# Kernel tuning notes

Hardware: AMD Instinct MI355X
Metric: run time of the kernel (lower is better)

The kernel has to match this reference:

```python
import jax, jax.numpy as jnp
import numpy as np

B, QL, KVL = 2, 1024, 2048
D = 4096          # hidden_size
NH, NKV = 32, 8   # attention heads / kv heads
HD = D // NH      # head_dim = 128
INNER = 4 * D     # SwiGLU intermediate = 16384
EPS = 1e-5
THETA = 10000.0


def rope_cos_sin(seq_len, head_dim, theta):
    inv_freq = 1.0 / (theta ** (jnp.arange(0, head_dim, 2, dtype=jnp.float32) / head_dim))
    t = jnp.arange(seq_len, dtype=jnp.float32)
    freqs = jnp.outer(t, inv_freq)                      # [S, HD/2]
    emb = jnp.concatenate([freqs, freqs], axis=-1)      # [S, HD]
    return jnp.cos(emb), jnp.sin(emb)


def rotate_half(x):
    half = x.shape[-1] // 2
    return jnp.concatenate([-x[..., half:], x[..., :half]], axis=-1)


def apply_rope(x, cos, sin):
    # x: [B, H, S, HD]; cos/sin: [S, HD] broadcast over batch & heads
    return x * cos[None, None] + rotate_half(x) * sin[None, None]


def layernorm(x, w, b):
    mu = jnp.mean(x, axis=-1, keepdims=True)
    var = jnp.var(x, axis=-1, keepdims=True)
    return (x - mu) * jax.lax.rsqrt(var + EPS) * w + b


def setup_inputs() -> dict:
    key = jax.random.key(0)
    ks = jax.random.split(key, 12)
    s = 0.02
    return {
        "hidden_states": jax.random.normal(ks[0], (B, QL, D), jnp.float32),
        "encoder_hidden_states": jax.random.normal(ks[1], (B, KVL, D), jnp.float32),
        "encoder_attention_mask": jnp.ones((B, KVL), jnp.float32),
        "ln1_w": jnp.ones((D,), jnp.float32),
        "ln1_b": jnp.zeros((D,), jnp.float32),
        "q_w": jax.random.normal(ks[2], (D, D), jnp.float32) * s,        # [out, in]
        "k_w": jax.random.normal(ks[3], (NKV * HD, D), jnp.float32) * s,
        "v_w": jax.random.normal(ks[4], (NKV * HD, D), jnp.float32) * s,
        "o_w": jax.random.normal(ks[5], (D, D), jnp.float32) * s,
        "ln2_w": jnp.ones((D,), jnp.float32),
        "ln2_b": jnp.zeros((D,), jnp.float32),
        "gate_w": jax.random.normal(ks[6], (INNER, D), jnp.float32) * s,
        "up_w": jax.random.normal(ks[7], (INNER, D), jnp.float32) * s,
        "down_w": jax.random.normal(ks[8], (D, INNER), jnp.float32) * s,
    }


def reference(hidden_states, encoder_hidden_states, encoder_attention_mask,
              ln1_w, ln1_b, q_w, k_w, v_w, o_w, ln2_w, ln2_b,
              gate_w, up_w, down_w):
    residual = hidden_states
    h = layernorm(hidden_states, ln1_w, ln1_b)

    # projections
    q = (h @ q_w.T).reshape(B, QL, NH, HD).transpose(0, 2, 1, 3)                    # [B,NH,QL,HD]
    k = (encoder_hidden_states @ k_w.T).reshape(B, KVL, NKV, HD).transpose(0, 2, 1, 3)  # [B,NKV,KVL,HD]
    v = (encoder_hidden_states @ v_w.T).reshape(B, KVL, NKV, HD).transpose(0, 2, 1, 3)

    # RoPE: q uses positions 0..QL-1, k uses positions 0..KVL-1 (position_ids=None -> cos[None])
    q_cos, q_sin = rope_cos_sin(QL, HD, THETA)
    kv_cos, kv_sin = rope_cos_sin(KVL, HD, THETA)
    q = apply_rope(q, q_cos, q_sin)
    k = apply_rope(k, kv_cos, kv_sin)

    # GQA repeat_kv: each kv head repeated num_key_value_groups times consecutively
    n_rep = NH // NKV
    k = jnp.repeat(k, n_rep, axis=1)  # [B,NH,KVL,HD]
    v = jnp.repeat(v, n_rep, axis=1)

    attn = jnp.einsum('bhqd,bhkd->bhqk', q, k) / np.sqrt(HD).astype(np.float32)
    # NOTE: original code ADDS the boolean mask (True -> +1.0) to the logits
    mask = (encoder_attention_mask != 0).astype(attn.dtype)  # [B,KVL]
    attn = attn + mask[:, None, None, :]
    attn = jax.nn.softmax(attn.astype(jnp.float32), axis=-1).astype(q.dtype)

    out = jnp.einsum('bhqk,bhkd->bhqd', attn, v)        # [B,NH,QL,HD]
    out = out.transpose(0, 2, 1, 3).reshape(B, QL, D)
    attn_out = out @ o_w.T

    h = residual + attn_out
    residual = h
    h = layernorm(h, ln2_w, ln2_b)
    ff = (jax.nn.silu(h @ gate_w.T) * (h @ up_w.T)) @ down_w.T
    return residual + ff
```

## Files before the change

### kernel.cpp

```cpp
#include <hip/hip_runtime.h>
#include <hip/hip_bf16.h>
#include <math.h>

using bf16 = __hip_bfloat16;
typedef __bf16 bfv8 __attribute__((ext_vector_type(8)));
typedef float f32x4 __attribute__((ext_vector_type(4)));

__device__ __forceinline__ f32x4 mfma16(bfv8 a, bfv8 b, f32x4 c) {
    return __builtin_amdgcn_mfma_f32_16x16x32_bf16(a, b, c, 0, 0, 0);
}

__device__ __forceinline__ void gload_lds16(const void* g, void* l) {
    __builtin_amdgcn_global_load_lds(
        (const __attribute__((address_space(1))) void*)g,
        (__attribute__((address_space(3))) void*)l, 16, 0, 0);
}

__global__ void cvt_kernel(const float* __restrict__ in, bf16* __restrict__ out, long n8) {
    long u = (long)blockIdx.x * 256 + threadIdx.x;
    if (u >= n8) return;
    const float4* p = (const float4*)in + u * 2;
    float4 a = p[0], b = p[1];
    bf16 t8[8] = { __float2bfloat16(a.x), __float2bfloat16(a.y), __float2bfloat16(a.z), __float2bfloat16(a.w),
                   __float2bfloat16(b.x), __float2bfloat16(b.y), __float2bfloat16(b.z), __float2bfloat16(b.w) };
    *(int4*)(out + u * 8) = *(const int4*)t8;
}

__global__ void layernorm_kernel(const float* __restrict__ x, const float* __restrict__ gw,
                                 const float* __restrict__ gb, bf16* __restrict__ out)
{
    const int D = 4096;
    int row = blockIdx.x, t = threadIdx.x;
    const float4* xr = (const float4*)(x + (size_t)row * D);
    float4 v[4];
    float s1 = 0.f, s2 = 0.f;
#pragma unroll
    for (int j = 0; j < 4; ++j) {
        v[j] = xr[t + j * 256];
        s1 += v[j].x + v[j].y + v[j].z + v[j].w;
        s2 += v[j].x * v[j].x + v[j].y * v[j].y + v[j].z * v[j].z + v[j].w * v[j].w;
    }
#pragma unroll
    for (int d = 1; d < 64; d <<= 1) { s1 += __shfl_xor(s1, d); s2 += __shfl_xor(s2, d); }
    __shared__ float red[8];
    int wave = t >> 6, lane = t & 63;
    if (lane == 0) { red[wave] = s1; red[4 + wave] = s2; }
    __syncthreads();
    s1 = red[0] + red[1] + red[2] + red[3];
    s2 = red[4] + red[5] + red[6] + red[7];
    float mu = s1 * (1.f / 4096.f);
    float var = s2 * (1.f / 4096.f) - mu * mu;
    float rs = rsqrtf(var + 1e-5f);
    bf16* orow = out + (size_t)row * D;
#pragma unroll
    for (int j = 0; j < 4; ++j) {
        int base = (t + j * 256) * 4;
        float xs[4] = { v[j].x, v[j].y, v[j].z, v[j].w };
        bf16 o4[4];
#pragma unroll
        for (int c = 0; c < 4; ++c)
            o4[c] = __float2bfloat16((xs[c] - mu) * rs * gw[base + c] + gb[base + c]);
        *(int2*)(orow + base) = *(const int2*)o4;
    }
}

__global__ void rope_kernel(bf16* __restrict__ x, int nheads, int seqlen, long total) {
    long idx = (long)blockIdx.x * 256 + threadIdx.x;
    if (idx >= total) return;
    int j = (int)(idx & 63);
    long t2 = idx >> 6;
    int h = (int)(t2 % nheads);
    long row = t2 / nheads;
    int pos = (int)(row % seqlen);
    float inv = exp2f(-(float)j * 0.20762050593046015f);
    float ang = (float)pos * inv;
    float s, c;
    sincosf(ang, &s, &c);
    bf16* p = x + row * ((long)nheads * 128) + (long)h * 128 + j;
    float x0 = __bfloat162float(p[0]);
    float x1 = __bfloat162float(p[64]);
    p[0]  = __float2bfloat16(x0 * c - x1 * s);
    p[64] = __float2bfloat16(x1 * c + x0 * s);
}

template<int BM, int BN, int MODE, bool DUAL, int CM, int CN, int XN>
__global__ __launch_bounds__(512, 2) void gemm_p(
        const bf16* __restrict__ A, const bf16* __restrict__ W, const bf16* __restrict__ W2,
        void* __restrict__ Cout, void* __restrict__ Cout2, const void* __restrict__ aux,
        int M, int N, int K, int Nsplit)
{
    constexpr int MF = BM / 32;
    constexpr int NF = BN / 64;
    constexpr int ALD = BM / 128;
    constexpr int BLD = BN / 128;
    constexpr int SLD = ALD + BLD;
    __shared__ bf16 lds[3][(BM + BN) * 32];

    const int t = threadIdx.x;
    const int wid = t >> 6, lane = t & 63;
    const int lr = lane & 15, lg = lane >> 4;
    const int wr = wid >> 2, wc = wid & 3;
    const int bid = blockIdx.x;
    const int xcd = bid & 7, slot = bid >> 3;
    const int sm = slot / CN, sn = slot % CN;
    const int xm = xcd / XN, xn = xcd % XN;
    const int bm = (xm * CM + sm) * BM;
    const int bn = (xn * CN + sn) * BN;

    auto stage = [&](int tt, int buf) {
        const int k0 = tt * 32;
        char* ldsA = (char*)&lds[buf][0];
#pragma unroll
        for (int c = 0; c < ALD; ++c) {
            int Wb = (t + c * 512) * 16;
            int L = Wb ^ (((Wb >> 7) & 7) << 4);
            int row = L >> 6, colb = L & 63;
            gload_lds16(A + (size_t)(bm + row) * K + k0 + (colb >> 1), ldsA + Wb);
        }
        char* ldsB = (char*)&lds[buf][BM * 32];
#pragma unroll
        for (int c = 0; c < BLD; ++c) {
            int Wb = (t + c * 512) * 16;
            int L = Wb ^ (((Wb >> 7) & 7) << 4);
            int row = L >> 6, colb = L & 63;
            const bf16* src;
            if constexpr (DUAL) {
                int nr = bn + row;
                src = (nr >= Nsplit) ? W2 + (size_t)(nr - Nsplit) * K + k0 + (colb >> 1)
                                     : W  + (size_t)nr * K + k0 + (colb >> 1);
            } else {
                src = W + (size_t)(bn + row) * K + k0 + (colb >> 1);
            }
            gload_lds16(src, ldsB + Wb);
        }
    };

    const f32x4 zero4 = { 0.f, 0.f, 0.f, 0.f };
    f32x4 acc[MF][NF];
#pragma unroll
    for (int m = 0; m < MF; ++m)
#pragma unroll
        for (int n = 0; n < NF; ++n) acc[m][n] = zero4;

    const int T = K >> 5;
    stage(0, 0);
    stage(1, 1);
    if constexpr (SLD == 4) asm volatile("s_waitcnt vmcnt(4)" ::: "memory");
    else                    asm volatile("s_waitcnt vmcnt(3)" ::: "memory");
    __builtin_amdgcn_s_barrier();
    __builtin_amdgcn_sched_barrier(0);

    for (int tt = 0; tt < T; ++tt) {
        const int buf = tt % 3;
        bfv8 af[MF], bfr[NF];
#pragma unroll
        for (int m = 0; m < MF; ++m) {
            int row = wr * (BM / 2) + m * 16 + lr;
            int U = row * 64 + lg * 16;
            af[m] = *(const bfv8*)((const char*)&lds[buf][0] + (U ^ (((U >> 7) & 7) << 4)));
        }
#pragma unroll
        for (int n = 0; n < NF; ++n) {
            int row = wc * (BN / 4) + n * 16 + lr;
            int U = row * 64 + lg * 16;
            bfr[n] = *(const bfv8*)((const char*)&lds[buf][BM * 32] + (U ^ (((U >> 7) & 7) << 4)));
        }
        if (tt + 2 < T) stage(tt + 2, (tt + 2) % 3);
        __builtin_amdgcn_s_setprio(1);
#pragma unroll
        for (int m = 0; m < MF; ++m)
#pragma unroll
            for (int n = 0; n < NF; ++n)
                acc[m][n] = mfma16(af[m], bfr[n], acc[m][n]);
        __builtin_amdgcn_s_setprio(0);
        if (tt + 2 < T) {
            if constexpr (SLD == 4) asm volatile("s_waitcnt vmcnt(4)" ::: "memory");
            else                    asm volatile("s_waitcnt vmcnt(3)" ::: "memory");
        } else {
            asm volatile("s_waitcnt vmcnt(0)" ::: "memory");
        }
        __builtin_amdgcn_s_barrier();
        __builtin_amdgcn_sched_barrier(0);
    }

    const int r0 = bm + wr * (BM / 2), c0 = bn + wc * (BN / 4);
#pragma unroll
    for (int m = 0; m < MF; ++m)
#pragma unroll
        for (int n = 0; n < NF; ++n)
#pragma unroll
            for (int i = 0; i < 4; ++i) {
                int r = r0 + m * 16 + lg * 4 + i;
                int c = c0 + n * 16 + lr;
                float a = acc[m][n][i];
                if constexpr (DUAL) {
                    if (c < Nsplit) ((bf16*)Cout)[(size_t)r * Nsplit + c] = __float2bfloat16(a);
                    else ((bf16*)Cout2)[(size_t)r * (N - Nsplit) + (c - Nsplit)] = __float2bfloat16(a);
                } else {
                    size_t idx = (size_t)r * N + c;
                    if constexpr (MODE == 0) {
                        ((bf16*)Cout)[idx] = __float2bfloat16(a);
                    } else if constexpr (MODE == 1) {
                        a = a / (1.f + expf(-a));
                        ((bf16*)Cout)[idx] = __float2bfloat16(a);
                    } else if constexpr (MODE == 2) {
                        a *= __bfloat162float(((const bf16*)aux)[idx]);
                        ((bf16*)Cout)[idx] = __float2bfloat16(a);
                    } else {
                        ((float*)Cout)[idx] = a + ((const float*)aux)[idx];
                    }
                }
            }
}

__global__ void transpose_v(const bf16* __restrict__ vb, bf16* __restrict__ vt) {
    __shared__ bf16 tile[64][68];
    int kv0 = blockIdx.x * 64, c0 = blockIdx.y * 64, b = blockIdx.z;
    int t = threadIdx.x;
    int cr = t & 15, rr = t >> 4;
#pragma unroll
    for (int j = 0; j < 4; ++j) {
        int r = rr + j * 16;
        *(int2*)&tile[r][cr * 4] = *(const int2*)&vb[(size_t)(b * 2048 + kv0 + r) * 1024 + c0 + cr * 4];
    }
    __syncthreads();
#pragma unroll
    for (int j = 0; j < 4; ++j) {
        int cc = rr + j * 16;
        bf16 tmp[4];
#pragma unroll
        for (int q = 0; q < 4; ++q) tmp[q] = tile[cr * 4 + q][cc];
        *(int2*)&vt[(size_t)(b * 1024 + c0 + cc) * 2048 + kv0 + cr * 4] = *(const int2*)tmp;
    }
}

__global__ __launch_bounds__(256) void attn_kernel(
    const bf16* __restrict__ Q, const bf16* __restrict__ Kb, const bf16* __restrict__ Vt,
    const float* __restrict__ mask, bf16* __restrict__ O)
{
    const int QL_ = 1024, KVL_ = 2048;
    const float scale = 0.08838834764831845f;
    int qt = blockIdx.x, h = blockIdx.y, b = blockIdx.z;
    int t = threadIdx.x, wave = t >> 6, lane = t & 63;
    int lr = lane & 15, lg = lane >> 4;
    int g = h >> 2;
    __shared__ bf16 Ksm[64 * 128];
    __shared__ bf16 Vsm[128 * 64];
    __shared__ bf16 Psm[4][16 * 72];
    int q0 = qt * 64 + wave * 16;

    const bf16* qptr = Q + (size_t)(b * QL_ + q0 + lr) * 4096 + h * 128;
    bfv8 qf[4];
#pragma unroll
    for (int kc = 0; kc < 4; ++kc) qf[kc] = *(const bfv8*)(qptr + kc * 32 + lg * 8);

    const f32x4 zero4 = { 0.f, 0.f, 0.f, 0.f };
    f32x4 accO[8];
#pragma unroll
    for (int dt = 0; dt < 8; ++dt) accO[dt] = zero4;
    float mrow[4] = { -1e30f, -1e30f, -1e30f, -1e30f };
    float lrow[4] = { 0.f, 0.f, 0.f, 0.f };

    for (int kv0 = 0; kv0 < KVL_; kv0 += 64) {
#pragma unroll
        for (int p2 = 0; p2 < 4; ++p2) {
            int Wb = (p2 * 256 + t) * 16;
            int row = Wb >> 8;
            int col = ((Wb & 255) ^ ((row & 7) << 4)) >> 1;
            gload_lds16(Kb + (size_t)(b * KVL_ + kv0 + row) * 1024 + g * 128 + col,
                        (char*)Ksm + Wb);
        }
#pragma unroll
        for (int p2 = 0; p2 < 4; ++p2) {
            int Wb = (p2 * 256 + t) * 16;
            int row = Wb >> 7;
            int col = ((Wb & 127) ^ ((row & 7) << 4)) >> 1;
            gload_lds16(Vt + (size_t)(b * 1024 + g * 128 + row) * 2048 + kv0 + col,
                        (char*)Vsm + Wb);
        }
        __syncthreads();

        f32x4 s[4];
#pragma unroll
        for (int ct = 0; ct < 4; ++ct) {
            s[ct] = zero4;
#pragma unroll
            for (int kc = 0; kc < 4; ++kc) {
                int row = ct * 16 + lr;
                int U = row * 256 + kc * 64 + lg * 16;
                bfv8 kf = *(const bfv8*)((const char*)Ksm + (U ^ ((row & 7) << 4)));
                s[ct] = mfma16(qf[kc], kf, s[ct]);
            }
            float mv = mask[(size_t)b * KVL_ + kv0 + ct * 16 + lr];
            mv = (mv != 0.f) ? 1.f : 0.f;
#pragma unroll
            for (int i = 0; i < 4; ++i) s[ct][i] = s[ct][i] * scale + mv;
        }

        float rmx[4], mnew[4], corr[4], psum[4];
#pragma unroll
        for (int i = 0; i < 4; ++i) {
            rmx[i] = fmaxf(fmaxf(s[0][i], s[1][i]), fmaxf(s[2][i], s[3][i]));
#pragma unroll
            for (int d = 1; d < 16; d <<= 1) rmx[i] = fmaxf(rmx[i], __shfl_xor(rmx[i], d));
            mnew[i] = fmaxf(mrow[i], rmx[i]);
            corr[i] = expf(mrow[i] - mnew[i]);
            psum[i] = 0.f;
        }
#pragma unroll
        for (int ct = 0; ct < 4; ++ct)
#pragma unroll
            for (int i = 0; i < 4; ++i) {
                float pv = expf(s[ct][i] - mnew[i]);
                psum[i] += pv;
                Psm[wave][(lg * 4 + i) * 72 + ct * 16 + lr] = __float2bfloat16(pv);
            }
#pragma unroll
        for (int i = 0; i < 4; ++i) {
#pragma unroll
            for (int d = 1; d < 16; d <<= 1) psum[i] += __shfl_xor(psum[i], d);
            lrow[i] = lrow[i] * corr[i] + psum[i];
            mrow[i] = mnew[i];
        }
#pragma unroll
        for (int dt = 0; dt < 8; ++dt)
#pragma unroll
            for (int i = 0; i < 4; ++i) accO[dt][i] *= corr[i];
        __syncthreads();

        bfv8 pf0 = *(const bfv8*)&Psm[wave][lr * 72 + 0 * 32 + lg * 8];
        bfv8 pf1 = *(const bfv8*)&Psm[wave][lr * 72 + 1 * 32 + lg * 8];
#pragma unroll
        for (int dt = 0; dt < 8; ++dt) {
            int row = dt * 16 + lr;
            int U0 = row * 128 + 0 * 64 + lg * 16;
            int U1 = row * 128 + 1 * 64 + lg * 16;
            bfv8 vf0 = *(const bfv8*)((const char*)Vsm + (U0 ^ ((row & 7) << 4)));
            bfv8 vf1 = *(const bfv8*)((const char*)Vsm + (U1 ^ ((row & 7) << 4)));
            accO[dt] = mfma16(pf0, vf0, accO[dt]);
            accO[dt] = mfma16(pf1, vf1, accO[dt]);
        }
        __syncthreads();
    }

    float invl[4];
#pragma unroll
    for (int i = 0; i < 4; ++i) invl[i] = 1.f / lrow[i];
#pragma unroll
    for (int dt = 0; dt < 8; ++dt)
#pragma unroll
        for (int i = 0; i < 4; ++i)
            O[(size_t)(b * QL_ + q0 + lg * 4 + i) * 4096 + h * 128 + dt * 16 + lr] =
                __float2bfloat16(accO[dt][i] * invl[i]);
}

extern "C" void kernel_launch(void* const* d_in, const int* in_sizes, int n_in,
                              void* d_out, int out_size, void* d_ws, size_t ws_size,
                              hipStream_t stream) {
    const float* hidden = (const float*)d_in[0];
    const float* enc    = (const float*)d_in[1];
    const float* mask   = (const float*)d_in[2];
    const float* ln1w   = (const float*)d_in[3];
    const float* ln1b   = (const float*)d_in[4];
    const float* qw     = (const float*)d_in[5];
    const float* kw     = (const float*)d_in[6];
    const float* vw     = (const float*)d_in[7];
    const float* ow     = (const float*)d_in[8];
    const float* ln2w   = (const float*)d_in[9];
    const float* ln2b   = (const float*)d_in[10];
    const float* gatew  = (const float*)d_in[11];
    const float* upw    = (const float*)d_in[12];
    const float* downw  = (const float*)d_in[13];
    float* out = (float*)d_out;

    char* ws = (char*)d_ws;
    bf16*  wbuf  = (bf16*)(ws);
    bf16*  wbuf2 = (bf16*)(ws + 8388608);
    bf16*  h1    = (bf16*)(ws + 134217728);
    bf16*  encb  = (bf16*)(ws + 150994944);
    bf16*  qb    = (bf16*)(ws + 184549376);
    bf16*  kb    = (bf16*)(ws + 201326592);
    bf16*  vb    = (bf16*)(ws + 209715200);
    bf16*  attno = (bf16*)(ws + 218103808);
    float* h2    = (float*)(ws + 234881024);
    bf16*  vt    = (bf16*)(ws + 234881024);
    bf16*  h2n   = (bf16*)(ws + 268435456);
    bf16*  g1    = (bf16*)(ws + 285212672);

    auto cvt = [&](const float* src, bf16* dst, long n) {
        cvt_kernel<<<(int)(n / 2048), 256, 0, stream>>>(src, dst, n / 8);
    };

    cvt(enc, encb, 16777216L);
    layernorm_kernel<<<2048, 256, 0, stream>>>(hidden, ln1w, ln1b, h1);

    cvt(qw, wbuf, 16777216L);
    gemm_p<128, 256, 0, false, 8, 4, 4><<<256, 512, 0, stream>>>(
        h1, wbuf, nullptr, qb, nullptr, nullptr, 2048, 4096, 4096, 0);
    rope_kernel<<<16384, 256, 0, stream>>>(qb, 32, 1024, 2048L * 32 * 64);

    cvt(kw, wbuf, 4194304L);
    cvt(vw, wbuf2, 4194304L);
    gemm_p<128, 256, 0, true, 8, 4, 2><<<256, 512, 0, stream>>>(
        encb, wbuf, wbuf2, kb, vb, nullptr, 4096, 2048, 4096, 1024);
    rope_kernel<<<8192, 256, 0, stream>>>(kb, 8, 2048, 4096L * 8 * 64);
    transpose_v<<<dim3(32, 16, 2), 256, 0, stream>>>(vb, vt);

    attn_kernel<<<dim3(16, 32, 2), 256, 0, stream>>>(qb, kb, vt, mask, attno);

    cvt(ow, wbuf, 16777216L);
    gemm_p<128, 256, 3, false, 8, 4, 4><<<256, 512, 0, stream>>>(
        attno, wbuf, nullptr, h2, nullptr, hidden, 2048, 4096, 4096, 0);

    layernorm_kernel<<<2048, 256, 0, stream>>>(h2, ln2w, ln2b, h2n);

    cvt(gatew, wbuf, 67108864L);
    gemm_p<256, 256, 1, false, 8, 8, 8><<<512, 512, 0, stream>>>(
        h2n, wbuf, nullptr, g1, nullptr, nullptr, 2048, 16384, 4096, 0);
    cvt(upw, wbuf, 67108864L);
    gemm_p<256, 256, 2, false, 8, 8, 8><<<512, 512, 0, stream>>>(
        h2n, wbuf, nullptr, g1, nullptr, g1, 2048, 16384, 4096, 0);

    cvt(downw, wbuf, 67108864L);
    gemm_p<128, 256, 3, false, 8, 4, 4><<<256, 512, 0, stream>>>(
        g1, wbuf, nullptr, out, nullptr, h2, 2048, 4096, 16384, 0);
}
```

Before: 1.574 ms.

## Replace GEMM with 256-row, K=64 double-buffered 8-wave ping-pong schedule

Rewrites the bf16 MFMA GEMM into a kernel with fixed 256-row M tiles and 64-wide K steps in two LDS buffers. Each K step is split into four quadrant phases, with LDS fragment loads interleaved between barrier-separated MFMA bursts, and the next stage is prefetched mid-iteration. The aim is to overlap LDS reads and global loads with matrix math and to cut per-K-step barrier overhead. In exchange it uses more registers and LDS, drops occupancy to one block per CU, and changes the tile-to-block mapping, so the 128-BN launches now cover 256 rows per block.

```diff
diff --git a/kernel.cpp b/kernel.cpp
--- a/kernel.cpp
+++ b/kernel.cpp
@@ -83,18 +83,18 @@
     p[64] = __float2bfloat16(x1 * c + x0 * s);
 }
 
-template<int BM, int BN, int MODE, bool DUAL, int CM, int CN, int XN>
-__global__ __launch_bounds__(512, 2) void gemm_p(
+template<int BN, int MODE, bool DUAL, int CM, int CN, int XN>
+__global__ __launch_bounds__(512, 1) void gemm8(
         const bf16* __restrict__ A, const bf16* __restrict__ W, const bf16* __restrict__ W2,
         void* __restrict__ Cout, void* __restrict__ Cout2, const void* __restrict__ aux,
         int M, int N, int K, int Nsplit)
 {
-    constexpr int MF = BM / 32;
-    constexpr int NF = BN / 64;
-    constexpr int ALD = BM / 128;
-    constexpr int BLD = BN / 128;
-    constexpr int SLD = ALD + BLD;
-    __shared__ bf16 lds[3][(BM + BN) * 32];
+    constexpr int NFH = BN / 128;
+    constexpr int ABY = 256 * 128;
+    constexpr int BBY = BN * 128;
+    constexpr int BLD = BN / 64;
+    constexpr int SLD = 4 + BLD;
+    __shared__ alignas(16) char lds8[2][ABY + BBY];
 
     const int t = threadIdx.x;
     const int wid = t >> 6, lane = t & 63;
@@ -104,95 +104,132 @@
     const int xcd = bid & 7, slot = bid >> 3;
     const int sm = slot / CN, sn = slot % CN;
     const int xm = xcd / XN, xn = xcd % XN;
-    const int bm = (xm * CM + sm) * BM;
+    const int bm = (xm * CM + sm) * 256;
     const int bn = (xn * CN + sn) * BN;
 
-    auto stage = [&](int tt, int buf) {
-        const int k0 = tt * 32;
-        char* ldsA = (char*)&lds[buf][0];
-#pragma unroll
-        for (int c = 0; c < ALD; ++c) {
+    auto stage = [&](int kt, int b) {
+        const int k0 = kt * 64;
+        char* base = &lds8[b][0];
+#pragma unroll
+        for (int c = 0; c < 4; ++c) {
             int Wb = (t + c * 512) * 16;
             int L = Wb ^ (((Wb >> 7) & 7) << 4);
-            int row = L >> 6, colb = L & 63;
-            gload_lds16(A + (size_t)(bm + row) * K + k0 + (colb >> 1), ldsA + Wb);
-        }
-        char* ldsB = (char*)&lds[buf][BM * 32];
+            gload_lds16(A + (size_t)(bm + (L >> 7)) * K + k0 + ((L & 127) >> 1), base + Wb);
+        }
 #pragma unroll
         for (int c = 0; c < BLD; ++c) {
             int Wb = (t + c * 512) * 16;
             int L = Wb ^ (((Wb >> 7) & 7) << 4);
-            int row = L >> 6, colb = L & 63;
             const bf16* src;
             if constexpr (DUAL) {
-                int nr = bn + row;
-                src = (nr >= Nsplit) ? W2 + (size_t)(nr - Nsplit) * K + k0 + (colb >> 1)
-                                     : W  + (size_t)nr * K + k0 + (colb >> 1);
+                int nr = bn + (L >> 7);
+                src = (nr >= Nsplit) ? W2 + (size_t)(nr - Nsplit) * K + k0 + ((L & 127) >> 1)
+                                     : W  + (size_t)nr * K + k0 + ((L & 127) >> 1);
             } else {
-                src = W + (size_t)(bn + row) * K + k0 + (colb >> 1);
+                src = W + (size_t)(bn + (L >> 7)) * K + k0 + ((L & 127) >> 1);
             }
-            gload_lds16(src, ldsB + Wb);
+            gload_lds16(src, base + ABY + Wb);
         }
     };
 
     const f32x4 zero4 = { 0.f, 0.f, 0.f, 0.f };
-    f32x4 acc[MF][NF];
-#pragma unroll
-    for (int m = 0; m < MF; ++m)
-#pragma unroll
-        for (int n = 0; n < NF; ++n) acc[m][n] = zero4;
-
-    const int T = K >> 5;
+    f32x4 acc[8][2 * NFH];
+#pragma unroll
+    for (int m = 0; m < 8; ++m)
+#pragma unroll
+        for (int n = 0; n < 2 * NFH; ++n) acc[m][n] = zero4;
+
+    bfv8 af[4][2], bfr[2][NFH][2];
+
+#define LOADA(B, MH) do {                                                     \
+    const char* _ba = &lds8[B][0];                                            \
+    _Pragma("unroll") for (int m = 0; m < 4; ++m)                             \
+    _Pragma("unroll") for (int ks = 0; ks < 2; ++ks) {                        \
+        int row = wr * 128 + (MH) * 64 + m * 16 + lr;                         \
+        int U = row * 128 + ks * 64 + lg * 16;                                \
+        af[m][ks] = *(const bfv8*)(_ba + (U ^ ((row & 7) << 4)));             \
+    } } while (0)
+
+#define LOADB(B, NH) do {                                                     \
+    const char* _bb = &lds8[B][ABY];                                          \
+    _Pragma("unroll") for (int n = 0; n < NFH; ++n)                           \
+    _Pragma("unroll") for (int ks = 0; ks < 2; ++ks) {                        \
+        int row = wc * (BN / 4) + (NH) * (BN / 8) + n * 16 + lr;              \
+        int U = row * 128 + ks * 64 + lg * 16;                                \
+        bfr[NH][n][ks] = *(const bfv8*)(_bb + (U ^ ((row & 7) << 4)));        \
+    } } while (0)
+
+#define MFMAQ(MH, NH) do {                                                    \
+    _Pragma("unroll") for (int m = 0; m < 4; ++m)                             \
+    _Pragma("unroll") for (int n = 0; n < NFH; ++n) {                         \
+        acc[(MH)*4+m][(NH)*NFH+n] = mfma16(af[m][0], bfr[NH][n][0], acc[(MH)*4+m][(NH)*NFH+n]); \
+        acc[(MH)*4+m][(NH)*NFH+n] = mfma16(af[m][1], bfr[NH][n][1], acc[(MH)*4+m][(NH)*NFH+n]); \
+    } } while (0)
+
+#define PH_TOP() do { __builtin_amdgcn_sched_barrier(0); __builtin_amdgcn_s_barrier();       \
+    asm volatile("s_waitcnt lgkmcnt(0)" ::: "memory"); __builtin_amdgcn_sched_barrier(0);    \
+    __builtin_amdgcn_s_setprio(1); } while (0)
+
+#define PH_END() do { __builtin_amdgcn_s_setprio(0); __builtin_amdgcn_sched_barrier(0);      \
+    __builtin_amdgcn_s_barrier(); } while (0)
+
+#define VM_PRE() do { if constexpr (SLD == 8) asm volatile("s_waitcnt vmcnt(8)" ::: "memory"); \
+                      else asm volatile("s_waitcnt vmcnt(6)" ::: "memory"); } while (0)
+
+    const int T = K >> 6;
+    const int T2 = T >> 1;
+
     stage(0, 0);
     stage(1, 1);
-    if constexpr (SLD == 4) asm volatile("s_waitcnt vmcnt(4)" ::: "memory");
-    else                    asm volatile("s_waitcnt vmcnt(3)" ::: "memory");
+    VM_PRE();
+    __builtin_amdgcn_sched_barrier(0);
     __builtin_amdgcn_s_barrier();
-    __builtin_amdgcn_sched_barrier(0);
-
-    for (int tt = 0; tt < T; ++tt) {
-        const int buf = tt % 3;
-        bfv8 af[MF], bfr[NF];
-#pragma unroll
-        for (int m = 0; m < MF; ++m) {
-            int row = wr * (BM / 2) + m * 16 + lr;
-            int U = row * 64 + lg * 16;
-            af[m] = *(const bfv8*)((const char*)&lds[buf][0] + (U ^ (((U >> 7) & 7) << 4)));
-        }
-#pragma unroll
-        for (int n = 0; n < NF; ++n) {
-            int row = wc * (BN / 4) + n * 16 + lr;
-            int U = row * 64 + lg * 16;
-            bfr[n] = *(const bfv8*)((const char*)&lds[buf][BM * 32] + (U ^ (((U >> 7) & 7) << 4)));
-        }
-        if (tt + 2 < T) stage(tt + 2, (tt + 2) % 3);
-        __builtin_amdgcn_s_setprio(1);
-#pragma unroll
-        for (int m = 0; m < MF; ++m)
-#pragma unroll
-            for (int n = 0; n < NF; ++n)
-                acc[m][n] = mfma16(af[m], bfr[n], acc[m][n]);
+
+    for (int tt = 0; tt < T2; ++tt) {
+        const bool pre = (tt + 1 < T2);
+        LOADA(0, 0); LOADB(0, 0);
+        PH_TOP(); MFMAQ(0, 0); PH_END();
+        LOADB(0, 1);
+        PH_TOP(); MFMAQ(0, 1); PH_END();
+        LOADA(0, 1);
+        PH_TOP(); MFMAQ(1, 1); PH_END();
+        if (pre) stage(2 * tt + 2, 0);
+        PH_TOP(); MFMAQ(1, 0);
         __builtin_amdgcn_s_setprio(0);
-        if (tt + 2 < T) {
-            if constexpr (SLD == 4) asm volatile("s_waitcnt vmcnt(4)" ::: "memory");
-            else                    asm volatile("s_waitcnt vmcnt(3)" ::: "memory");
-        } else {
-            asm volatile("s_waitcnt vmcnt(0)" ::: "memory");
-        }
+        if (pre) { VM_PRE(); } else { asm volatile("s_waitcnt vmcnt(0)" ::: "memory"); }
+        __builtin_amdgcn_sched_barrier(0);
         __builtin_amdgcn_s_barrier();
+        LOADA(1, 0); LOADB(1, 0);
+        PH_TOP(); MFMAQ(0, 0); PH_END();
+        LOADB(1, 1);
+        PH_TOP(); MFMAQ(0, 1); PH_END();
+        LOADA(1, 1);
+        PH_TOP(); MFMAQ(1, 1); PH_END();
+        if (pre) stage(2 * tt + 3, 1);
+        PH_TOP(); MFMAQ(1, 0);
+        __builtin_amdgcn_s_setprio(0);
+        if (pre) { VM_PRE(); }
         __builtin_amdgcn_sched_barrier(0);
-    }
-
-    const int r0 = bm + wr * (BM / 2), c0 = bn + wc * (BN / 4);
-#pragma unroll
-    for (int m = 0; m < MF; ++m)
-#pragma unroll
-        for (int n = 0; n < NF; ++n)
+        __builtin_amdgcn_s_barrier();
+    }
+
+#undef LOADA
+#undef LOADB
+#undef MFMAQ
+#undef PH_TOP
+#undef PH_END
+#undef VM_PRE
+
+    const int r0 = bm + wr * 128, c0 = bn + wc * (BN / 4);
+#pragma unroll
+    for (int mg = 0; mg < 8; ++mg)
+#pragma unroll
+        for (int ng = 0; ng < 2 * NFH; ++ng)
 #pragma unroll
             for (int i = 0; i < 4; ++i) {
-                int r = r0 + m * 16 + lg * 4 + i;
-                int c = c0 + n * 16 + lr;
-                float a = acc[m][n][i];
+                int r = r0 + mg * 16 + lg * 4 + i;
+                int c = c0 + ng * 16 + lr;
+                float a = acc[mg][ng][i];
                 if constexpr (DUAL) {
                     if (c < Nsplit) ((bf16*)Cout)[(size_t)r * Nsplit + c] = __float2bfloat16(a);
                     else ((bf16*)Cout2)[(size_t)r * (N - Nsplit) + (c - Nsplit)] = __float2bfloat16(a);
@@ -395,13 +432,13 @@
     layernorm_kernel<<<2048, 256, 0, stream>>>(hidden, ln1w, ln1b, h1);
 
     cvt(qw, wbuf, 16777216L);
-    gemm_p<128, 256, 0, false, 8, 4, 4><<<256, 512, 0, stream>>>(
+    gemm8<128, 0, false, 8, 4, 8><<<256, 512, 0, stream>>>(
         h1, wbuf, nullptr, qb, nullptr, nullptr, 2048, 4096, 4096, 0);
     rope_kernel<<<16384, 256, 0, stream>>>(qb, 32, 1024, 2048L * 32 * 64);
 
     cvt(kw, wbuf, 4194304L);
     cvt(vw, wbuf2, 4194304L);
-    gemm_p<128, 256, 0, true, 8, 4, 2><<<256, 512, 0, stream>>>(
+    gemm8<128, 0, true, 8, 4, 4><<<256, 512, 0, stream>>>(
         encb, wbuf, wbuf2, kb, vb, nullptr, 4096, 2048, 4096, 1024);
     rope_kernel<<<8192, 256, 0, stream>>>(kb, 8, 2048, 4096L * 8 * 64);
     transpose_v<<<dim3(32, 16, 2), 256, 0, stream>>>(vb, vt);
@@ -409,19 +446,19 @@
     attn_kernel<<<dim3(16, 32, 2), 256, 0, stream>>>(qb, kb, vt, mask, attno);
 
     cvt(ow, wbuf, 16777216L);
-    gemm_p<128, 256, 3, false, 8, 4, 4><<<256, 512, 0, stream>>>(
+    gemm8<128, 3, false, 8, 4, 8><<<256, 512, 0, stream>>>(
         attno, wbuf, nullptr, h2, nullptr, hidden, 2048, 4096, 4096, 0);
 
     layernorm_kernel<<<2048, 256, 0, stream>>>(h2, ln2w, ln2b, h2n);
 
     cvt(gatew, wbuf, 67108864L);
-    gemm_p<256, 256, 1, false, 8, 8, 8><<<512, 512, 0, stream>>>(
+    gemm8<256, 1, false, 8, 8, 8><<<512, 512, 0, stream>>>(
         h2n, wbuf, nullptr, g1, nullptr, nullptr, 2048, 16384, 4096, 0);
     cvt(upw, wbuf, 67108864L);
-    gemm_p<256, 256, 2, false, 8, 8, 8><<<512, 512, 0, stream>>>(
+    gemm8<256, 2, false, 8, 8, 8><<<512, 512, 0, stream>>>(
         h2n, wbuf, nullptr, g1, nullptr, g1, 2048, 16384, 4096, 0);
 
     cvt(downw, wbuf, 67108864L);
-    gemm_p<128, 256, 3, false, 8, 4, 4><<<256, 512, 0, stream>>>(
+    gemm8<128, 3, false, 8, 4, 8><<<256, 512, 0, stream>>>(
         g1, wbuf, nullptr, out, nullptr, h2, 2048, 4096, 16384, 0);
 }
```

Measured after the change: 1.627 ms. +3.3%, slower.

## Add 8-wave ping-pong pipelined GEMM kernel for FFN projections

Applied to the files above, without the earlier changes.

Introduces a new gemm8 kernel that splits each K-tile into quarter phases. In each phase, LDS fragment loads and global-to-LDS prefetches are interleaved with MFMA bursts, using barriers, s_setprio and explicit vmcnt gates. It uses double buffering for 256-wide N tiles and triple buffering for 128-wide tiles, with swizzled LDS addresses. It replaces gemm_p for the gate, up and down projections, and the down projection also gets a different XCD block mapping (XN changes from 4 to 8). The goal is better overlap of memory traffic with matrix-core work in the dominant FFN GEMMs, at the cost of complex hand-scheduled synchronisation.

```diff
diff --git a/kernel.cpp b/kernel.cpp
--- a/kernel.cpp
+++ b/kernel.cpp
@@ -213,6 +213,193 @@
             }
 }
 
+template<int BN, int MODE, bool DUAL, int CM, int CN, int XN>
+__global__ __launch_bounds__(512, 1) void gemm8(
+        const bf16* __restrict__ A, const bf16* __restrict__ W, const bf16* __restrict__ W2,
+        void* __restrict__ Cout, void* __restrict__ Cout2, const void* __restrict__ aux,
+        int M, int N, int K, int Nsplit)
+{
+    constexpr bool BIG = (BN == 256);
+    constexpr int NBUF = BIG ? 2 : 3;
+    constexpr int ABY = 32768;
+    constexpr int BBY = BN * 128;
+    constexpr int TBY = ABY + BBY;
+    __shared__ alignas(16) char lds8[NBUF * TBY];
+
+    const int t = threadIdx.x;
+    const int wid = t >> 6, lane = t & 63;
+    const int lr = lane & 15, lg = lane >> 4;
+    const int wr = wid >> 2, wc = wid & 3;
+    const int bid = blockIdx.x;
+    const int xcd = bid & 7, slot = bid >> 3;
+    const int sm = slot / CN, sn = slot % CN;
+    const int xm = xcd / XN, xn = xcd % XN;
+    const int bm = (xm * CM + sm) * 256;
+    const int bn = (xn * CN + sn) * BN;
+
+    auto stA = [&](int kt, int h, int buf) {
+#pragma unroll
+        for (int c = 0; c < 2; ++c) {
+            int Wb = (t + c * 512) * 16;
+            int L = Wb ^ (((Wb >> 7) & 7) << 4);
+            gload_lds16(A + (size_t)(bm + h * 128 + (L >> 7)) * K + kt * 64 + ((L & 127) >> 1),
+                        lds8 + buf * TBY + h * 16384 + Wb);
+        }
+    };
+    auto stB = [&](int kt, int h, int buf) {
+#pragma unroll
+        for (int c = 0; c < 2; ++c) {
+            int Wb = (t + c * 512) * 16;
+            int L = Wb ^ (((Wb >> 7) & 7) << 4);
+            int nr = bn + h * 128 + (L >> 7);
+            const bf16* src;
+            if constexpr (DUAL) {
+                src = (nr >= Nsplit) ? W2 + (size_t)(nr - Nsplit) * K + kt * 64 + ((L & 127) >> 1)
+                                     : W  + (size_t)nr * K + kt * 64 + ((L & 127) >> 1);
+            } else {
+                src = W + (size_t)nr * K + kt * 64 + ((L & 127) >> 1);
+            }
+            gload_lds16(src, lds8 + buf * TBY + ABY + h * 16384 + Wb);
+        }
+    };
+
+    const f32x4 zero4 = { 0.f, 0.f, 0.f, 0.f };
+    f32x4 acc[8][BIG ? 4 : 2];
+#pragma unroll
+    for (int m = 0; m < 8; ++m)
+#pragma unroll
+        for (int n = 0; n < (BIG ? 4 : 2); ++n) acc[m][n] = zero4;
+
+    bfv8 af[4][2], bfr[BIG ? 2 : 1][2][2];
+
+#define LOADA(BUF, MH) do {                                                   \
+    const char* _ba = lds8 + (BUF) * TBY;                                     \
+    _Pragma("unroll") for (int m = 0; m < 4; ++m)                             \
+    _Pragma("unroll") for (int ks = 0; ks < 2; ++ks) {                        \
+        int row = wr * 128 + (MH) * 64 + m * 16 + lr;                         \
+        int U = row * 128 + ks * 64 + lg * 16;                                \
+        af[m][ks] = *(const bfv8*)(_ba + (U ^ ((row & 7) << 4)));             \
+    } } while (0)
+
+#define LOADB(BUF, NH) do {                                                   \
+    const char* _bb = lds8 + (BUF) * TBY + ABY;                               \
+    _Pragma("unroll") for (int n = 0; n < 2; ++n)                             \
+    _Pragma("unroll") for (int ks = 0; ks < 2; ++ks) {                        \
+        int row = wc * (BN / 4) + (NH) * (BN / 8) + n * 16 + lr;              \
+        int U = row * 128 + ks * 64 + lg * 16;                                \
+        bfr[NH][n][ks] = *(const bfv8*)(_bb + (U ^ ((row & 7) << 4)));        \
+    } } while (0)
+
+#define MFMAQ(MH, NH) do {                                                    \
+    _Pragma("unroll") for (int m = 0; m < 4; ++m)                             \
+    _Pragma("unroll") for (int n = 0; n < 2; ++n) {                           \
+        acc[(MH)*4+m][(NH)*2+n] = mfma16(af[m][0], bfr[NH][n][0], acc[(MH)*4+m][(NH)*2+n]); \
+        acc[(MH)*4+m][(NH)*2+n] = mfma16(af[m][1], bfr[NH][n][1], acc[(MH)*4+m][(NH)*2+n]); \
+    } } while (0)
+
+#define PH_TOP() do { __builtin_amdgcn_s_barrier();                           \
+    asm volatile("s_waitcnt lgkmcnt(0)" ::: "memory");                        \
+    __builtin_amdgcn_sched_barrier(0);                                        \
+    __builtin_amdgcn_s_setprio(1); } while (0)
+
+#define PH_END() do { __builtin_amdgcn_s_setprio(0);                          \
+    __builtin_amdgcn_s_barrier(); } while (0)
+
+#define GATE(LIVE) do { __builtin_amdgcn_s_setprio(0);                        \
+    if (LIVE) { if constexpr (BIG) asm volatile("s_waitcnt vmcnt(4)" ::: "memory"); \
+                else               asm volatile("s_waitcnt vmcnt(6)" ::: "memory"); } \
+    else      asm volatile("s_waitcnt vmcnt(0)" ::: "memory");                \
+    __builtin_amdgcn_s_barrier(); } while (0)
+
+    const int T = K >> 6;
+    const int T2 = T >> 1;
+
+    if constexpr (BIG) {
+        stA(0, 0, 0); stA(0, 1, 0); stB(0, 0, 0); stB(0, 1, 0);
+        stB(1, 0, 1); stB(1, 1, 1);
+        asm volatile("s_waitcnt vmcnt(4)" ::: "memory");
+        __builtin_amdgcn_s_barrier();
+
+        for (int tt = 0; tt < T2; ++tt) {
+            const int o = 2 * tt + 1, e2 = 2 * tt + 2, o2 = 2 * tt + 3;
+            const bool le = (e2 < T), lo = (o2 < T);
+            LOADA(0, 0); LOADB(0, 0); stA(o, 0, 1);
+            PH_TOP(); MFMAQ(0, 0); PH_END();
+            LOADB(0, 1); stA(o, 1, 1);
+            PH_TOP(); MFMAQ(0, 1); PH_END();
+            LOADA(0, 1); if (le) stB(e2, 0, 0);
+            PH_TOP(); MFMAQ(1, 1); PH_END();
+            if (le) stB(e2, 1, 0);
+            PH_TOP(); MFMAQ(1, 0); GATE(le);
+            LOADA(1, 0); LOADB(1, 0); if (le) stA(e2, 0, 0);
+            PH_TOP(); MFMAQ(0, 0); PH_END();
+            LOADB(1, 1); if (le) stA(e2, 1, 0);
+            PH_TOP(); MFMAQ(0, 1); PH_END();
+            LOADA(1, 1); if (lo) stB(o2, 0, 1);
+            PH_TOP(); MFMAQ(1, 1); PH_END();
+            if (lo) stB(o2, 1, 1);
+            PH_TOP(); MFMAQ(1, 0); GATE(le);
+        }
+    } else {
+        stA(0, 0, 0); stB(0, 0, 0); stA(0, 1, 0);
+        stA(1, 0, 1); stB(1, 0, 1); stA(1, 1, 1);
+        asm volatile("s_waitcnt vmcnt(6)" ::: "memory");
+        __builtin_amdgcn_s_barrier();
+
+        int bE = 0, bO = 1, bN = 2;
+        for (int tt = 0; tt < T2; ++tt) {
+            const int e2 = 2 * tt + 2, o2 = 2 * tt + 3;
+            const bool le = (e2 < T), lo = (o2 < T);
+            LOADA(bE, 0); LOADB(bE, 0); if (le) { stA(e2, 0, bN); stB(e2, 0, bN); }
+            PH_TOP(); MFMAQ(0, 0); PH_END();
+            LOADA(bE, 1); if (le) stA(e2, 1, bN);
+            PH_TOP(); MFMAQ(1, 0); GATE(le);
+            LOADA(bO, 0); LOADB(bO, 0); if (lo) { stA(o2, 0, bE); stB(o2, 0, bE); }
+            PH_TOP(); MFMAQ(0, 0); PH_END();
+            LOADA(bO, 1); if (lo) stA(o2, 1, bE);
+            PH_TOP(); MFMAQ(1, 0); GATE(lo);
+            int nE = bN, nO = bE, nN = bO;
+            bE = nE; bO = nO; bN = nN;
+        }
+    }
+
+#undef LOADA
+#undef LOADB
+#undef MFMAQ
+#undef PH_TOP
+#undef PH_END
+#undef GATE
+
+    const int r0 = bm + wr * 128, c0 = bn + wc * (BN / 4);
+#pragma unroll
+    for (int mg = 0; mg < 8; ++mg)
+#pragma unroll
+        for (int ng = 0; ng < (BIG ? 4 : 2); ++ng)
+#pragma unroll
+            for (int i = 0; i < 4; ++i) {
+                int r = r0 + mg * 16 + lg * 4 + i;
+                int c = c0 + ng * 16 + lr;
+                float a = acc[mg][ng][i];
+                if constexpr (DUAL) {
+                    if (c < Nsplit) ((bf16*)Cout)[(size_t)r * Nsplit + c] = __float2bfloat16(a);
+                    else ((bf16*)Cout2)[(size_t)r * (N - Nsplit) + (c - Nsplit)] = __float2bfloat16(a);
+                } else {
+                    size_t idx = (size_t)r * N + c;
+                    if constexpr (MODE == 0) {
+                        ((bf16*)Cout)[idx] = __float2bfloat16(a);
+                    } else if constexpr (MODE == 1) {
+                        a = a / (1.f + expf(-a));
+                        ((bf16*)Cout)[idx] = __float2bfloat16(a);
+                    } else if constexpr (MODE == 2) {
+                        a *= __bfloat162float(((const bf16*)aux)[idx]);
+                        ((bf16*)Cout)[idx] = __float2bfloat16(a);
+                    } else {
+                        ((float*)Cout)[idx] = a + ((const float*)aux)[idx];
+                    }
+                }
+            }
+}
+
 __global__ void transpose_v(const bf16* __restrict__ vb, bf16* __restrict__ vt) {
     __shared__ bf16 tile[64][68];
     int kv0 = blockIdx.x * 64, c0 = blockIdx.y * 64, b = blockIdx.z;
@@ -415,13 +602,13 @@
     layernorm_kernel<<<2048, 256, 0, stream>>>(h2, ln2w, ln2b, h2n);
 
     cvt(gatew, wbuf, 67108864L);
-    gemm_p<256, 256, 1, false, 8, 8, 8><<<512, 512, 0, stream>>>(
+    gemm8<256, 1, false, 8, 8, 8><<<512, 512, 0, stream>>>(
         h2n, wbuf, nullptr, g1, nullptr, nullptr, 2048, 16384, 4096, 0);
     cvt(upw, wbuf, 67108864L);
-    gemm_p<256, 256, 2, false, 8, 8, 8><<<512, 512, 0, stream>>>(
+    gemm8<256, 2, false, 8, 8, 8><<<512, 512, 0, stream>>>(
         h2n, wbuf, nullptr, g1, nullptr, g1, 2048, 16384, 4096, 0);
 
     cvt(downw, wbuf, 67108864L);
-    gemm_p<128, 256, 3, false, 8, 4, 4><<<256, 512, 0, stream>>>(
+    gemm8<128, 3, false, 8, 4, 8><<<256, 512, 0, stream>>>(
         g1, wbuf, nullptr, out, nullptr, h2, 2048, 4096, 16384, 0);
 }
```

New measurement: 1.490 ms. -5.3%, faster.
